# Optimization experiments

Hardware: AMD Instinct MI355X
Metric: run time of the kernel (lower is better)

The kernel has to match this reference:

```python
import jax, jax.numpy as jnp
import numpy as np

N = 100000   # nodes
E = 3200000  # edges
CY = 128     # channels_y (signal length per node)
HID = 10     # hidden_channels
H = 2        # heads
C = 10       # out channels per head
BN_EPS = 1e-5


def _glorot(k, shape):
    lim = float(np.sqrt(6.0 / (shape[0] + shape[1])))
    return jax.random.uniform(k, shape, jnp.float32, -lim, lim)


def setup_inputs() -> dict:
    key = jax.random.key(0)
    ks = jax.random.split(key, 16)
    p = {}
    p["signal"] = jax.random.normal(ks[0], (N, CY), jnp.float32)
    p["edge_index"] = jax.random.randint(ks[1], (2, E), 0, N)
    p["edge_weight"] = jax.random.uniform(ks[2], (E,), jnp.float32)
    p["mask"] = jax.random.bernoulli(ks[3], 0.3, (N,))
    # mlp_in: Linear(CY,512) -> BatchNorm -> ReLU -> Linear(512,HID) (PyG MLP, plain_last)
    p["W1"] = _glorot(ks[4], (CY, 512)); p["b1"] = jnp.zeros((512,), jnp.float32)
    p["gamma"] = jnp.ones((512,), jnp.float32); p["beta"] = jnp.zeros((512,), jnp.float32)
    p["W2"] = _glorot(ks[5], (512, HID)); p["b2"] = jnp.zeros((HID,), jnp.float32)
    # GATv2Conv(HID, HID, heads=2, edge_dim=1, concat=True)
    p["Wl"] = _glorot(ks[6], (HID, H * C)); p["bl"] = jnp.zeros((H * C,), jnp.float32)
    p["Wr"] = _glorot(ks[7], (HID, H * C)); p["br"] = jnp.zeros((H * C,), jnp.float32)
    p["We"] = _glorot(ks[8], (1, H * C))              # lin_edge, no bias
    p["att"] = _glorot(ks[9], (H, C))                 # attention vector per head
    p["gat_bias"] = jnp.zeros((H * C,), jnp.float32)
    # mlp_out: MLP([20,512]) single layer, plain_last -> just Linear (dropout off in eval)
    p["W3"] = _glorot(ks[10], (H * C, 512)); p["b3"] = jnp.zeros((512,), jnp.float32)
    # out_linear: Linear(512, CY)
    p["W4"] = _glorot(ks[11], (512, CY)); p["b4"] = jnp.zeros((CY,), jnp.float32)
    return p


def _forward(signal, edge_index, edge_weight, mask,
             W1, b1, gamma, beta, W2, b2,
             Wl, bl, Wr, br, We, att, gat_bias,
             W3, b3, W4, b4):
    # node masking: (signal.T * ~mask).T
    x = signal * (~mask)[:, None].astype(signal.dtype)
    # mlp_in (eval mode: BN with running mean=0, var=1)
    x = x @ W1 + b1
    x = x * (gamma / jnp.sqrt(jnp.asarray(1.0 + BN_EPS, x.dtype))) + beta
    x = jax.nn.relu(x)
    x = x @ W2 + b2                                   # [N, HID]
    # GATv2Conv
    src, dst = edge_index[0], edge_index[1]
    xl = (x @ Wl + bl).reshape(N, H, C)               # source transform
    xr = (x @ Wr + br).reshape(N, H, C)               # target transform
    ea = (edge_weight[:, None] @ We).reshape(E, H, C)  # edge feature transform
    e = jax.nn.leaky_relu(xl[src] + xr[dst] + ea, 0.2)  # [E,H,C]
    alpha = jnp.einsum('ehc,hc->eh', e, att)          # [E,H]
    # segment softmax over incoming edges of each dst node
    m = jax.ops.segment_max(alpha, dst, num_segments=N)
    ex = jnp.exp(alpha - m[dst])
    den = jax.ops.segment_sum(ex, dst, num_segments=N)
    a = ex / (den[dst] + 1e-16)                       # [E,H]
    out = jax.ops.segment_sum(xl[src] * a[:, :, None], dst, num_segments=N)
    out = out.reshape(N, H * C) + gat_bias            # concat heads + bias
    # mlp_out (single plain-last layer) + out_linear
    out = out @ W3 + b3
    out = out @ W4 + b4
    return out


def reference(signal, edge_index, edge_weight, mask,
              W1, b1, gamma, beta, W2, b2,
              Wl, bl, Wr, br, We, att, gat_bias,
              W3, b3, W4, b4):
    return _forward(signal, edge_index, edge_weight, mask,
                    W1, b1, gamma, beta, W2, b2,
                    Wl, bl, Wr, br, We, att, gat_bias,
                    W3, b3, W4, b4)
```

## Files before the change

### kernel.cpp

```cpp
#include <hip/hip_runtime.h>
#include <hip/hip_bf16.h>

constexpr int NN = 100000;
constexpr int NE = 3200000;
constexpr int CYC = 128;
constexpr int NB = 1563;
constexpr int EBLK = 256;
constexpr int ECHUNK = NE / EBLK;
constexpr int MSCAN = NB * EBLK;
constexpr int CAP = 2432;
constexpr int NBLK_A = (NN + 63) / 64;

#define OFF_W1T    0u
#define OFF_W2T    131072u
#define OFF_B1E    147456u
#define OFF_SMALL  149504u
#define OFF_W34    151808u
#define OFF_B34    162048u
#define OFF_FLAGS  162560u
#define OFF_XLB    163840u
#define OFF_XR     6563840u
#define OFF_GH     14563840u
#define OFF_BB     16164352u
#define OFF_BS     16170752u
#define OFF_BIN    16171776u

#define SF_WLR 0
#define SF_BLR 400
#define SF_ATT 440
#define SF_WE  460
#define SF_GB  480
#define SF_B2  500

typedef __attribute__((ext_vector_type(8))) short bf16x8;
typedef __attribute__((ext_vector_type(4))) float f32x4;

__device__ __forceinline__ float bfu(unsigned short x) {
  return __uint_as_float(((unsigned)x) << 16);
}
__device__ __forceinline__ short f2bf(float f) {
  __hip_bfloat16 h = __float2bfloat16(f);
  return *reinterpret_cast<short*>(&h);
}
__device__ __forceinline__ float LD(const void* p, long i, int f32f) {
  return f32f ? ((const float*)p)[i] : bfu(((const unsigned short*)p)[i]);
}

__global__ __launch_bounds__(256) void kPrep(
    const void* __restrict__ W1, const void* __restrict__ b1,
    const void* __restrict__ gamma, const void* __restrict__ beta,
    const void* __restrict__ W2, const void* __restrict__ b2,
    const void* __restrict__ Wl, const void* __restrict__ bl,
    const void* __restrict__ Wr, const void* __restrict__ br,
    const void* __restrict__ We, const void* __restrict__ att,
    const void* __restrict__ gbias, const void* __restrict__ W3,
    const void* __restrict__ b3, const void* __restrict__ W4,
    const void* __restrict__ b4, const void* __restrict__ mask,
    int* __restrict__ flags,
    short* __restrict__ W1T, float* __restrict__ b1eff, short* __restrict__ W2T,
    float* __restrict__ smallf, float* __restrict__ W34, float* __restrict__ b34)
{
  __shared__ int sfl[2];
  int t = threadIdx.x;
  if (t < 64) {
    const unsigned short* W1u = (const unsigned short*)W1;
    const unsigned* masku = (const unsigned*)mask;
    int big = 0;
#pragma unroll
    for (int k = 0; k < 8; k++) {
      unsigned e = (W1u[t * 8 + k] >> 7) & 0xFF;
      if (e >= 170) big++;
    }
    int byt = 0;
#pragma unroll
    for (int k = 0; k < 4; k++) if (masku[t * 4 + k] & ~1u) byt = 1;
#pragma unroll
    for (int o = 1; o < 64; o <<= 1) {
      big += __shfl_xor(big, o);
      byt |= __shfl_xor(byt, o);
    }
    if (t == 0) {
      sfl[0] = (big >= 4) ? 1 : 0;
      sfl[1] = byt;
      if (blockIdx.x == 0) { flags[0] = sfl[0]; flags[1] = byt; }
    }
  }
  __syncthreads();
  const int f32f = sfl[0];

  int tid = blockIdx.x * 256 + t;
  const float rs = 0.999995000037f;
  if (tid < 65536) {
    int j = tid >> 7, k = tid & 127;
    float s = LD(gamma, j, f32f) * rs;
    W1T[j * 128 + k] = f2bf(LD(W1, k * 512 + j, f32f) * s);
    if (k == 0) b1eff[j] = LD(b1, j, f32f) * s + LD(beta, j, f32f);
  } else if (tid < 73728) {
    int i = tid - 65536;
    int c = i >> 9, k = i & 511;
    W2T[c * 512 + k] = (c < 10) ? f2bf(LD(W2, k * 10 + c, f32f)) : (short)0;
  } else if (tid < 76288) {
    int i = tid - 73728;
    int j = i >> 7, tt = i & 127;
    float acc = 0.f;
    for (int k = 0; k < 512; k++) acc += LD(W3, j * 512 + k, f32f) * LD(W4, k * 128 + tt, f32f);
    W34[j * 128 + tt] = acc;
  } else if (tid < 76416) {
    int tt = tid - 76288;
    float acc = LD(b4, tt, f32f);
    for (int k = 0; k < 512; k++) acc += LD(b3, k, f32f) * LD(W4, k * 128 + tt, f32f);
    b34[tt] = acc;
  } else if (tid < 76932) {
    int i = tid - 76416;
    if (i < 400) {
      int c = i / 40, o = i % 40;
      smallf[SF_WLR + i] = (o < 20) ? LD(Wl, c * 20 + o, f32f) : LD(Wr, c * 20 + (o - 20), f32f);
    } else if (i < 440) {
      int o = i - 400;
      smallf[SF_BLR + o] = (o < 20) ? LD(bl, o, f32f) : LD(br, o - 20, f32f);
    } else if (i < 460) {
      smallf[SF_ATT + (i - 440)] = LD(att, i - 440, f32f);
    } else if (i < 480) {
      smallf[SF_WE + (i - 460)] = LD(We, i - 460, f32f);
    } else if (i < 500) {
      smallf[SF_GB + (i - 480)] = LD(gbias, i - 480, f32f);
    } else {
      int c = i - 500;
      smallf[SF_B2 + c] = (c < 10) ? LD(b2, c, f32f) : 0.f;
    }
  }
}

__global__ __launch_bounds__(256, 2) void kA(
    const void* __restrict__ sig, const void* __restrict__ mask,
    const short* __restrict__ W1T, const float* __restrict__ b1eff,
    const short* __restrict__ W2T, const float* __restrict__ smallf,
    const int* __restrict__ flags,
    unsigned short* __restrict__ xlb, float* __restrict__ xr)
{
  __shared__ __align__(16) char sR1[17408];
  __shared__ short sH[4][32 * 136];
  __shared__ float sb1[512];
  __shared__ float sxh[64][12];
  __shared__ float sWlr[400];
  __shared__ float sblr[40];
  __shared__ float sb2[16];

  short (*sA)[136]        = (short (*)[136])sR1;
  float (*sxhp)[64][17]   = (float (*)[64][17])sR1;
  float (*sxlr)[40]       = (float (*)[40])sR1;

  const int f32f = flags[0];
  const int mk8  = flags[1];
  int t = threadIdx.x;
  int w = t >> 6, l = t & 63;
  int lrow = l & 15, quad = l >> 4;
  int row0 = blockIdx.x * 64;

  for (int i = t; i < 512; i += 256) sb1[i] = b1eff[i];
  for (int i = t; i < 400; i += 256) sWlr[i] = smallf[SF_WLR + i];
  if (t < 40) sblr[t] = smallf[SF_BLR + t];
  if (t < 16) sb2[t] = smallf[SF_B2 + t];

  bf16x8 zz = {0, 0, 0, 0, 0, 0, 0, 0};
#pragma unroll
  for (int k = 0; k < 4; k++) {
    int idx = t + k * 256;
    int row = idx >> 4, seg = idx & 15;
    int gr = row0 + row;
    int grc = gr < NN ? gr : NN - 1;
    bool mbit = mk8 ? (((const unsigned char*)mask)[grc] != 0)
                    : (((const int*)mask)[grc] != 0);
    bf16x8 v;
    if (mbit) {
      v = zz;
    } else if (f32f) {
      const float4* Sf = (const float4*)((const float*)sig + (size_t)grc * CYC) + seg * 2;
      float4 x0 = Sf[0], x1 = Sf[1];
      v[0] = f2bf(x0.x); v[1] = f2bf(x0.y); v[2] = f2bf(x0.z); v[3] = f2bf(x0.w);
      v[4] = f2bf(x1.x); v[5] = f2bf(x1.y); v[6] = f2bf(x1.z); v[7] = f2bf(x1.w);
    } else {
      v = ((const bf16x8*)((const unsigned short*)sig + (size_t)grc * CYC))[seg];
    }
    *(bf16x8*)&sA[row][seg * 8] = v;
  }
  __syncthreads();

  float bcol[8];
#pragma unroll
  for (int ct = 0; ct < 8; ct++) bcol[ct] = sb1[w * 128 + ct * 16 + lrow];

  f32x4 acc[4][8];
#pragma unroll
  for (int rf = 0; rf < 4; rf++)
#pragma unroll
    for (int ct = 0; ct < 8; ct++) acc[rf][ct] = (f32x4){0.f, 0.f, 0.f, 0.f};

  const bf16x8* Bp = (const bf16x8*)W1T;
  int bvbase = w * 2048 + lrow * 16 + quad;
#pragma unroll
  for (int kt = 0; kt < 4; kt++) {
    bf16x8 a0 = *(const bf16x8*)&sA[lrow][kt * 32 + quad * 8];
    bf16x8 a1 = *(const bf16x8*)&sA[16 + lrow][kt * 32 + quad * 8];
    bf16x8 a2f = *(const bf16x8*)&sA[32 + lrow][kt * 32 + quad * 8];
    bf16x8 a3 = *(const bf16x8*)&sA[48 + lrow][kt * 32 + quad * 8];
#pragma unroll
    for (int ct = 0; ct < 8; ct++) {
      bf16x8 bv = Bp[bvbase + ct * 256 + kt * 4];
      acc[0][ct] = __builtin_amdgcn_mfma_f32_16x16x32_bf16(a0, bv, acc[0][ct], 0, 0, 0);
      acc[1][ct] = __builtin_amdgcn_mfma_f32_16x16x32_bf16(a1, bv, acc[1][ct], 0, 0, 0);
      acc[2][ct] = __builtin_amdgcn_mfma_f32_16x16x32_bf16(a2f, bv, acc[2][ct], 0, 0, 0);
      acc[3][ct] = __builtin_amdgcn_mfma_f32_16x16x32_bf16(a3, bv, acc[3][ct], 0, 0, 0);
    }
  }
  __syncthreads();

  const bf16x8* B2p = (const bf16x8*)W2T;
  bf16x8 b2v[4];
#pragma unroll
  for (int kt2 = 0; kt2 < 4; kt2++) b2v[kt2] = B2p[lrow * 64 + w * 16 + kt2 * 4 + quad];

  short* hb = &sH[w][0];
#pragma unroll
  for (int hf = 0; hf < 2; hf++) {
#pragma unroll
    for (int rr = 0; rr < 2; rr++) {
      int rf = hf * 2 + rr;
#pragma unroll
      for (int ct = 0; ct < 8; ct++) {
        float bb = bcol[ct];
#pragma unroll
        for (int r = 0; r < 4; r++) {
          float vv = fmaxf(acc[rf][ct][r] + bb, 0.f);
          hb[(rr * 16 + quad * 4 + r) * 136 + ct * 16 + lrow] = f2bf(vv);
        }
      }
    }
    asm volatile("s_waitcnt lgkmcnt(0)" ::: "memory");

    f32x4 a2[2];
    a2[0] = (f32x4){0.f, 0.f, 0.f, 0.f};
    a2[1] = (f32x4){0.f, 0.f, 0.f, 0.f};
#pragma unroll
    for (int kt2 = 0; kt2 < 4; kt2++) {
      bf16x8 x0 = *(const bf16x8*)&hb[lrow * 136 + kt2 * 32 + quad * 8];
      bf16x8 x1 = *(const bf16x8*)&hb[(16 + lrow) * 136 + kt2 * 32 + quad * 8];
      a2[0] = __builtin_amdgcn_mfma_f32_16x16x32_bf16(x0, b2v[kt2], a2[0], 0, 0, 0);
      a2[1] = __builtin_amdgcn_mfma_f32_16x16x32_bf16(x1, b2v[kt2], a2[1], 0, 0, 0);
    }
#pragma unroll
    for (int f = 0; f < 2; f++)
#pragma unroll
      for (int r = 0; r < 4; r++)
        sxhp[w][hf * 32 + f * 16 + quad * 4 + r][lrow] = a2[f][r];
  }
  __syncthreads();

  for (int i = t; i < 640; i += 256) {
    int row = i / 10, c = i - row * 10;
    sxh[row][c] = sxhp[0][row][c] + sxhp[1][row][c] + sxhp[2][row][c] + sxhp[3][row][c] + sb2[c];
  }
  __syncthreads();

  for (int i = t; i < 2560; i += 256) {
    int row = i / 40, o = i - row * 40;
    float v = sblr[o];
#pragma unroll
    for (int c = 0; c < 10; c++) v += sxh[row][c] * sWlr[c * 40 + o];
    sxlr[row][o] = v;
  }
  __syncthreads();

  int nrows = NN - row0; if (nrows > 64) nrows = 64;
  unsigned* xlb32 = (unsigned*)xlb;
#pragma unroll
  for (int k = 0; k < 4; k++) {
    int i = t + k * 256;
    int row = i >> 4, p = i & 15;
    if (row < nrows) {
      int s0 = 2 * p, s1 = 2 * p + 1;
      float lo = (s0 < 10) ? sxlr[row][s0] : (s0 >= 16 && s0 < 26) ? sxlr[row][s0 - 6] : 0.f;
      float hi = (s1 < 10) ? sxlr[row][s1] : (s1 >= 16 && s1 < 26) ? sxlr[row][s1 - 6] : 0.f;
      unsigned u = (unsigned)(unsigned short)f2bf(lo) |
                   ((unsigned)(unsigned short)f2bf(hi) << 16);
      xlb32[(size_t)(row0 + row) * 16 + p] = u;
    }
  }
#pragma unroll
  for (int k = 0; k < 5; k++) {
    int i = t + k * 256;
    int row = i / 20, c = i - row * 20;
    if (row < nrows) xr[(size_t)(row0 + row) * 20 + c] = sxlr[row][20 + c];
  }
}

__global__ __launch_bounds__(256) void kB1(const int* __restrict__ ei,
                                           int* __restrict__ gh) {
  __shared__ int h[NB];
  int t = threadIdx.x, blk = blockIdx.x;
  for (int i = t; i < NB; i += 256) h[i] = 0;
  __syncthreads();
  const int* dst = ei + NE;
  int base = blk * ECHUNK, bend = base + ECHUNK;
  for (int i = base + t; i < bend; i += 256)
    atomicAdd(&h[dst[i] >> 6], 1);
  __syncthreads();
  for (int i = t; i < NB; i += 256) gh[i * EBLK + blk] = h[i];
}

__global__ __launch_bounds__(256) void kS1(const int* __restrict__ gh,
                                           int* __restrict__ ghx,
                                           int* __restrict__ bsum) {
  __shared__ int sS[256];
  int t = threadIdx.x;
  int base = blockIdx.x * 2048 + t * 8;
  int d[8], tsum = 0;
#pragma unroll
  for (int k = 0; k < 8; k++) {
    d[k] = (base + k < MSCAN) ? gh[base + k] : 0;
    tsum += d[k];
  }
  sS[t] = tsum;
  __syncthreads();
  for (int o = 1; o < 256; o <<= 1) {
    int v = (t >= o) ? sS[t - o] : 0;
    __syncthreads();
    sS[t] += v;
    __syncthreads();
  }
  int run = sS[t] - tsum;
#pragma unroll
  for (int k = 0; k < 8; k++) {
    if (base + k < MSCAN) ghx[base + k] = run;
    run += d[k];
  }
  if (t == 255) bsum[blockIdx.x] = sS[255];
}

__global__ __launch_bounds__(256) void kS2(int* __restrict__ bsum, int nb) {
  __shared__ int sS[256];
  int t = threadIdx.x;
  int v = (t < nb) ? bsum[t] : 0;
  sS[t] = v;
  __syncthreads();
  for (int o = 1; o < 256; o <<= 1) {
    int u = (t >= o) ? sS[t - o] : 0;
    __syncthreads();
    sS[t] += u;
    __syncthreads();
  }
  if (t < nb) bsum[t] = sS[t] - v;
}

__global__ __launch_bounds__(256) void kS3(int* __restrict__ gh,
                                           const int* __restrict__ bsum,
                                           int* __restrict__ bb) {
  int i = blockIdx.x * 256 + threadIdx.x;
  int v = gh[i] + bsum[i >> 11];
  gh[i] = v;
  if ((i & 255) == 0) bb[i >> 8] = v;
  if (i == 0) bb[NB] = NE;
}

__global__ __launch_bounds__(256) void kB3(const int* __restrict__ ei,
                                           const void* __restrict__ ew,
                                           const int* __restrict__ flags,
                                           const int* __restrict__ gh,
                                           int2* __restrict__ binned) {
  __shared__ int cur[NB];
  const int f32f = flags[0];
  int t = threadIdx.x, blk = blockIdx.x;
  for (int i = t; i < NB; i += 256) cur[i] = gh[i * EBLK + blk];
  __syncthreads();
  int base = blk * ECHUNK, bend = base + ECHUNK;
  for (int i = base + t; i < bend; i += 256) {
    int s = ei[i], d = ei[NE + i];
    float w = LD(ew, i, f32f);
    int b = d >> 6;
    int pos = atomicAdd(&cur[b], 1);
    binned[pos] = make_int2(s | ((d & 63) << 17), __float_as_int(w));
  }
}

__global__ __launch_bounds__(256) void kSrtAgg(
    const int* __restrict__ bb, const int2* __restrict__ binned,
    const unsigned short* __restrict__ xlb, const float* __restrict__ xr,
    const float* __restrict__ smallf, const float* __restrict__ W34,
    const float* __restrict__ b34, const int* __restrict__ flags,
    void* __restrict__ out)
{
  __shared__ int2  sES[CAP];
  __shared__ float sXr[64 * 20];
  __shared__ float sW[2560];
  __shared__ int   sCnt[64];
  __shared__ int   sPre[64];
  __shared__ int   sStart[64];
  __shared__ int   sCur[64];
  __shared__ float sb[128];
  __shared__ float sAtt[20], sWe[20], sGb[20];

  const int f32f = flags[0];
  int t = threadIdx.x, b = blockIdx.x;
  int node0 = b * 64;

  for (int i = t; i < 2560; i += 256) sW[i] = W34[i];
  for (int i = t; i < 1280; i += 256) {
    int gi = node0 * 20 + i;
    sXr[i] = (gi < NN * 20) ? xr[gi] : 0.f;
  }
  if (t < 128) sb[t] = b34[t];
  if (t < 64) sCnt[t] = 0;
  if (t < 20) { sAtt[t] = smallf[SF_ATT + t]; sWe[t] = smallf[SF_WE + t]; sGb[t] = smallf[SF_GB + t]; }
  __syncthreads();

  int base = bb[b], end = bb[b + 1];
  int ne = end - base;

  for (int i = t; i < ne; i += 256)
    atomicAdd(&sCnt[(unsigned)binned[base + i].x >> 17], 1);
  __syncthreads();

  if (t < 64) sPre[t] = sCnt[t];
  __syncthreads();
  for (int o = 1; o < 64; o <<= 1) {
    int v = 0;
    if (t < 64 && t >= o) v = sPre[t - o];
    __syncthreads();
    if (t < 64) sPre[t] += v;
    __syncthreads();
  }
  if (t < 64) {
    int ex = sPre[t] - sCnt[t];
    sStart[t] = ex;
    sCur[t] = ex;
  }
  __syncthreads();

  for (int i = t; i < ne; i += 256) {
    int2 e = binned[base + i];
    int dl = (unsigned)e.x >> 17;
    int pos = atomicAdd(&sCur[dl], 1);
    if (pos < CAP) sES[pos] = make_int2(e.x & 0x1FFFF, e.y);
  }
  __syncthreads();

  int n = t >> 2, head = (t >> 1) & 1, part = t & 1;
  float xrw[10], attw[10], wew[10];
#pragma unroll
  for (int c = 0; c < 10; c++) {
    xrw[c]  = sXr[n * 20 + head * 10 + c];
    attw[c] = sAtt[head * 10 + c];
    wew[c]  = sWe[head * 10 + c];
  }
  float acc[10];
#pragma unroll
  for (int c = 0; c < 10; c++) acc[c] = 0.f;
  float den = 0.f;
  int s0 = sStart[n];
  int s1 = s0 + sCnt[n];
  if (s1 > CAP) s1 = CAP;
  for (int i = s0 + part; i < s1; i += 2) {
    int2 e = sES[i];
    const unsigned short* p = xlb + (size_t)e.x * 32 + head * 16;
    uint4 q = *(const uint4*)p;
    unsigned q4 = *(const unsigned*)(p + 8);
    float vl[10];
    unsigned qq[5] = {q.x, q.y, q.z, q.w, q4};
#pragma unroll
    for (int k = 0; k < 5; k++) {
      vl[2 * k]     = __uint_as_float(qq[k] << 16);
      vl[2 * k + 1] = __uint_as_float(qq[k] & 0xffff0000u);
    }
    float ww = __int_as_float(e.y);
    float a = 0.f;
#pragma unroll
    for (int c = 0; c < 10; c++) {
      float v = vl[c] + xrw[c] + ww * wew[c];
      v = fmaxf(v, 0.2f * v);
      a += v * attw[c];
    }
    float pp = __expf(a);
    den += pp;
#pragma unroll
    for (int c = 0; c < 10; c++) acc[c] += pp * vl[c];
  }
  den += __shfl_xor(den, 1);
#pragma unroll
  for (int c = 0; c < 10; c++) acc[c] += __shfl_xor(acc[c], 1);

  __syncthreads();
  if (part == 0) {
    float inv = 1.f / (den + 1e-16f);
#pragma unroll
    for (int c = 0; c < 10; c++)
      sXr[n * 20 + head * 10 + c] = acc[c] * inv + sGb[head * 10 + c];
  }
  __syncthreads();

  int col = t & 127, half = t >> 7;
  for (int n2 = half; n2 < 64; n2 += 2) {
    int gn = node0 + n2;
    if (gn >= NN) break;
    float v = sb[col];
    const float* g = &sXr[n2 * 20];
#pragma unroll
    for (int c = 0; c < 20; c++) v += g[c] * sW[c * 128 + col];
    if (f32f) ((float*)out)[(size_t)gn * 128 + col] = v;
    else ((unsigned short*)out)[(size_t)gn * 128 + col] = (unsigned short)f2bf(v);
  }
}

extern "C" void kernel_launch(void* const* d_in, const int* in_sizes, int n_in,
                              void* d_out, int out_size, void* d_ws, size_t ws_size,
                              hipStream_t stream) {
  (void)in_sizes; (void)n_in; (void)out_size; (void)ws_size;
  const void* sig  = d_in[0];
  const int*  ei   = (const int*)d_in[1];
  const void* ew   = d_in[2];
  const void* mask = d_in[3];
  const void* W1   = d_in[4];
  const void* b1   = d_in[5];
  const void* gam  = d_in[6];
  const void* bet  = d_in[7];
  const void* W2   = d_in[8];
  const void* b2   = d_in[9];
  const void* Wl   = d_in[10];
  const void* bl   = d_in[11];
  const void* Wr   = d_in[12];
  const void* br   = d_in[13];
  const void* We   = d_in[14];
  const void* att  = d_in[15];
  const void* gb   = d_in[16];
  const void* W3   = d_in[17];
  const void* b3   = d_in[18];
  const void* W4   = d_in[19];
  const void* b4   = d_in[20];

  char* ws = (char*)d_ws;
  short* W1T    = (short*)(ws + OFF_W1T);
  short* W2T    = (short*)(ws + OFF_W2T);
  float* b1eff  = (float*)(ws + OFF_B1E);
  float* smallf = (float*)(ws + OFF_SMALL);
  float* W34    = (float*)(ws + OFF_W34);
  float* b34    = (float*)(ws + OFF_B34);
  int*   flags  = (int*)(ws + OFF_FLAGS);
  unsigned short* xlb = (unsigned short*)(ws + OFF_XLB);
  float* xr     = (float*)(ws + OFF_XR);
  int*   gh     = (int*)(ws + OFF_GH);
  int*   bb     = (int*)(ws + OFF_BB);
  int*   bsum   = (int*)(ws + OFF_BS);
  int2*  bincsr = (int2*)(ws + OFF_BIN);

  kPrep<<<301, 256, 0, stream>>>(W1, b1, gam, bet, W2, b2, Wl, bl, Wr, br, We, att,
                                 gb, W3, b3, W4, b4, mask, flags,
                                 W1T, b1eff, W2T, smallf, W34, b34);
  kA<<<NBLK_A, 256, 0, stream>>>(sig, mask, W1T, b1eff, W2T, smallf, flags, xlb, xr);
  kB1<<<EBLK, 256, 0, stream>>>(ei, gh);
  kS1<<<(MSCAN + 2047) / 2048, 256, 0, stream>>>(gh, gh, bsum);
  kS2<<<1, 256, 0, stream>>>(bsum, (MSCAN + 2047) / 2048);
  kS3<<<NB, 256, 0, stream>>>(gh, bsum, bb);
  kB3<<<EBLK, 256, 0, stream>>>(ei, ew, flags, gh, bincsr);
  kSrtAgg<<<NB, 256, 0, stream>>>(bb, bincsr, xlb, xr, smallf, W34, b34, flags, d_out);
}
```

Measured before the change: 448.0 us.

## Build per-node CSR with global atomics instead of two-level bin sort

Replaces the block-bucketed histogram, scan and in-LDS per-node sort with a direct per-node global histogram, a scan over node counts, and a global-atomic scatter straight into per-node CSR order. The aggregation kernel then reads edges from global memory by node range, dropping the shared-memory re-sort and its CAP truncation. It also software-prefetches the next edge and its source features. The cost is heavy global atomic contention on per-node counters, and the scatter order within each node is no longer deterministic.

```diff
diff --git a/kernel.cpp b/kernel.cpp
--- a/kernel.cpp
+++ b/kernel.cpp
@@ -5,11 +5,8 @@
 constexpr int NE = 3200000;
 constexpr int CYC = 128;
 constexpr int NB = 1563;
-constexpr int EBLK = 256;
-constexpr int ECHUNK = NE / EBLK;
-constexpr int MSCAN = NB * EBLK;
-constexpr int CAP = 2432;
 constexpr int NBLK_A = (NN + 63) / 64;
+constexpr int NSCAN = 100352;
 
 #define OFF_W1T    0u
 #define OFF_W2T    131072u
@@ -20,8 +17,9 @@
 #define OFF_FLAGS  162560u
 #define OFF_XLB    163840u
 #define OFF_XR     6563840u
-#define OFF_GH     14563840u
-#define OFF_BB     16164352u
+#define OFF_NC     14563840u
+#define OFF_NS     14965248u
+#define OFF_NCU    15366656u
 #define OFF_BS     16170752u
 #define OFF_BIN    16171776u
 
@@ -58,7 +56,8 @@
     const void* __restrict__ b4, const void* __restrict__ mask,
     int* __restrict__ flags,
     short* __restrict__ W1T, float* __restrict__ b1eff, short* __restrict__ W2T,
-    float* __restrict__ smallf, float* __restrict__ W34, float* __restrict__ b34)
+    float* __restrict__ smallf, float* __restrict__ W34, float* __restrict__ b34,
+    int* __restrict__ ncnt)
 {
   __shared__ int sfl[2];
   int t = threadIdx.x;
@@ -89,6 +88,8 @@
   const int f32f = sfl[0];
 
   int tid = blockIdx.x * 256 + t;
+  if (tid < NSCAN) ncnt[tid] = 0;
+
   const float rs = 0.999995000037f;
   if (tid < 65536) {
     int j = tid >> 7, k = tid & 127;
@@ -294,30 +295,24 @@
   }
 }
 
-__global__ __launch_bounds__(256) void kB1(const int* __restrict__ ei,
-                                           int* __restrict__ gh) {
-  __shared__ int h[NB];
-  int t = threadIdx.x, blk = blockIdx.x;
-  for (int i = t; i < NB; i += 256) h[i] = 0;
-  __syncthreads();
+__global__ __launch_bounds__(256) void kHist(const int* __restrict__ ei,
+                                             int* __restrict__ ncnt) {
   const int* dst = ei + NE;
-  int base = blk * ECHUNK, bend = base + ECHUNK;
-  for (int i = base + t; i < bend; i += 256)
-    atomicAdd(&h[dst[i] >> 6], 1);
-  __syncthreads();
-  for (int i = t; i < NB; i += 256) gh[i * EBLK + blk] = h[i];
-}
-
-__global__ __launch_bounds__(256) void kS1(const int* __restrict__ gh,
-                                           int* __restrict__ ghx,
-                                           int* __restrict__ bsum) {
+  int stride = gridDim.x * 256;
+  for (int i = blockIdx.x * 256 + threadIdx.x; i < NE; i += stride)
+    atomicAdd(&ncnt[dst[i]], 1);
+}
+
+__global__ __launch_bounds__(256) void kS1(const int* __restrict__ in,
+                                           int* __restrict__ outx,
+                                           int* __restrict__ bsum, int nelem) {
   __shared__ int sS[256];
   int t = threadIdx.x;
   int base = blockIdx.x * 2048 + t * 8;
   int d[8], tsum = 0;
 #pragma unroll
   for (int k = 0; k < 8; k++) {
-    d[k] = (base + k < MSCAN) ? gh[base + k] : 0;
+    d[k] = (base + k < nelem) ? in[base + k] : 0;
     tsum += d[k];
   }
   sS[t] = tsum;
@@ -331,7 +326,7 @@
   int run = sS[t] - tsum;
 #pragma unroll
   for (int k = 0; k < 8; k++) {
-    if (base + k < MSCAN) ghx[base + k] = run;
+    if (base + k < nelem) outx[base + k] = run;
     run += d[k];
   }
   if (t == 255) bsum[blockIdx.x] = sS[255];
@@ -352,51 +347,43 @@
   if (t < nb) bsum[t] = sS[t] - v;
 }
 
-__global__ __launch_bounds__(256) void kS3(int* __restrict__ gh,
-                                           const int* __restrict__ bsum,
-                                           int* __restrict__ bb) {
+__global__ __launch_bounds__(256) void kS3n(int* __restrict__ nstart,
+                                            const int* __restrict__ bsum,
+                                            int* __restrict__ ncur, int nelem) {
   int i = blockIdx.x * 256 + threadIdx.x;
-  int v = gh[i] + bsum[i >> 11];
-  gh[i] = v;
-  if ((i & 255) == 0) bb[i >> 8] = v;
-  if (i == 0) bb[NB] = NE;
-}
-
-__global__ __launch_bounds__(256) void kB3(const int* __restrict__ ei,
-                                           const void* __restrict__ ew,
-                                           const int* __restrict__ flags,
-                                           const int* __restrict__ gh,
-                                           int2* __restrict__ binned) {
-  __shared__ int cur[NB];
+  if (i < nelem) {
+    int v = nstart[i] + bsum[i >> 11];
+    nstart[i] = v;
+    ncur[i] = v;
+  }
+}
+
+__global__ __launch_bounds__(256) void kB3n(const int* __restrict__ ei,
+                                            const void* __restrict__ ew,
+                                            const int* __restrict__ flags,
+                                            int* __restrict__ ncur,
+                                            int2* __restrict__ binned) {
   const int f32f = flags[0];
-  int t = threadIdx.x, blk = blockIdx.x;
-  for (int i = t; i < NB; i += 256) cur[i] = gh[i * EBLK + blk];
-  __syncthreads();
-  int base = blk * ECHUNK, bend = base + ECHUNK;
-  for (int i = base + t; i < bend; i += 256) {
+  int stride = gridDim.x * 256;
+  for (int i = blockIdx.x * 256 + threadIdx.x; i < NE; i += stride) {
     int s = ei[i], d = ei[NE + i];
     float w = LD(ew, i, f32f);
-    int b = d >> 6;
-    int pos = atomicAdd(&cur[b], 1);
-    binned[pos] = make_int2(s | ((d & 63) << 17), __float_as_int(w));
-  }
-}
-
-__global__ __launch_bounds__(256) void kSrtAgg(
-    const int* __restrict__ bb, const int2* __restrict__ binned,
+    int pos = atomicAdd(&ncur[d], 1);
+    binned[pos] = make_int2(s, __float_as_int(w));
+  }
+}
+
+__global__ __launch_bounds__(256) void kAgg(
+    const int* __restrict__ nstart, const int2* __restrict__ binned,
     const unsigned short* __restrict__ xlb, const float* __restrict__ xr,
     const float* __restrict__ smallf, const float* __restrict__ W34,
     const float* __restrict__ b34, const int* __restrict__ flags,
     void* __restrict__ out)
 {
-  __shared__ int2  sES[CAP];
   __shared__ float sXr[64 * 20];
   __shared__ float sW[2560];
-  __shared__ int   sCnt[64];
-  __shared__ int   sPre[64];
-  __shared__ int   sStart[64];
-  __shared__ int   sCur[64];
   __shared__ float sb[128];
+  __shared__ int   sStart[65];
   __shared__ float sAtt[20], sWe[20], sGb[20];
 
   const int f32f = flags[0];
@@ -409,39 +396,8 @@
     sXr[i] = (gi < NN * 20) ? xr[gi] : 0.f;
   }
   if (t < 128) sb[t] = b34[t];
-  if (t < 64) sCnt[t] = 0;
+  if (t < 65) sStart[t] = nstart[node0 + t];
   if (t < 20) { sAtt[t] = smallf[SF_ATT + t]; sWe[t] = smallf[SF_WE + t]; sGb[t] = smallf[SF_GB + t]; }
-  __syncthreads();
-
-  int base = bb[b], end = bb[b + 1];
-  int ne = end - base;
-
-  for (int i = t; i < ne; i += 256)
-    atomicAdd(&sCnt[(unsigned)binned[base + i].x >> 17], 1);
-  __syncthreads();
-
-  if (t < 64) sPre[t] = sCnt[t];
-  __syncthreads();
-  for (int o = 1; o < 64; o <<= 1) {
-    int v = 0;
-    if (t < 64 && t >= o) v = sPre[t - o];
-    __syncthreads();
-    if (t < 64) sPre[t] += v;
-    __syncthreads();
-  }
-  if (t < 64) {
-    int ex = sPre[t] - sCnt[t];
-    sStart[t] = ex;
-    sCur[t] = ex;
-  }
-  __syncthreads();
-
-  for (int i = t; i < ne; i += 256) {
-    int2 e = binned[base + i];
-    int dl = (unsigned)e.x >> 17;
-    int pos = atomicAdd(&sCur[dl], 1);
-    if (pos < CAP) sES[pos] = make_int2(e.x & 0x1FFFF, e.y);
-  }
   __syncthreads();
 
   int n = t >> 2, head = (t >> 1) & 1, part = t & 1;
@@ -456,14 +412,25 @@
 #pragma unroll
   for (int c = 0; c < 10; c++) acc[c] = 0.f;
   float den = 0.f;
-  int s0 = sStart[n];
-  int s1 = s0 + sCnt[n];
-  if (s1 > CAP) s1 = CAP;
-  for (int i = s0 + part; i < s1; i += 2) {
-    int2 e = sES[i];
+  int s0 = sStart[n], s1 = sStart[n + 1];
+
+  int i = s0 + part;
+  int2 e; uint4 q; unsigned q4;
+  if (i < s1) {
+    e = binned[i];
     const unsigned short* p = xlb + (size_t)e.x * 32 + head * 16;
-    uint4 q = *(const uint4*)p;
-    unsigned q4 = *(const unsigned*)(p + 8);
+    q = *(const uint4*)p;
+    q4 = *(const unsigned*)(p + 8);
+  }
+  while (i < s1) {
+    int j = i + 2;
+    int2 en; uint4 qn; unsigned qn4;
+    if (j < s1) {
+      en = binned[j];
+      const unsigned short* pn = xlb + (size_t)en.x * 32 + head * 16;
+      qn = *(const uint4*)pn;
+      qn4 = *(const unsigned*)(pn + 8);
+    }
     float vl[10];
     unsigned qq[5] = {q.x, q.y, q.z, q.w, q4};
 #pragma unroll
@@ -483,6 +450,7 @@
     den += pp;
 #pragma unroll
     for (int c = 0; c < 10; c++) acc[c] += pp * vl[c];
+    e = en; q = qn; q4 = qn4; i = j;
   }
   den += __shfl_xor(den, 1);
 #pragma unroll
@@ -546,19 +514,20 @@
   int*   flags  = (int*)(ws + OFF_FLAGS);
   unsigned short* xlb = (unsigned short*)(ws + OFF_XLB);
   float* xr     = (float*)(ws + OFF_XR);
-  int*   gh     = (int*)(ws + OFF_GH);
-  int*   bb     = (int*)(ws + OFF_BB);
+  int*   ncnt   = (int*)(ws + OFF_NC);
+  int*   nstart = (int*)(ws + OFF_NS);
+  int*   ncur   = (int*)(ws + OFF_NCU);
   int*   bsum   = (int*)(ws + OFF_BS);
   int2*  bincsr = (int2*)(ws + OFF_BIN);
 
-  kPrep<<<301, 256, 0, stream>>>(W1, b1, gam, bet, W2, b2, Wl, bl, Wr, br, We, att,
+  kPrep<<<392, 256, 0, stream>>>(W1, b1, gam, bet, W2, b2, Wl, bl, Wr, br, We, att,
                                  gb, W3, b3, W4, b4, mask, flags,
-                                 W1T, b1eff, W2T, smallf, W34, b34);
+                                 W1T, b1eff, W2T, smallf, W34, b34, ncnt);
+  kHist<<<2048, 256, 0, stream>>>(ei, ncnt);
   kA<<<NBLK_A, 256, 0, stream>>>(sig, mask, W1T, b1eff, W2T, smallf, flags, xlb, xr);
-  kB1<<<EBLK, 256, 0, stream>>>(ei, gh);
-  kS1<<<(MSCAN + 2047) / 2048, 256, 0, stream>>>(gh, gh, bsum);
-  kS2<<<1, 256, 0, stream>>>(bsum, (MSCAN + 2047) / 2048);
-  kS3<<<NB, 256, 0, stream>>>(gh, bsum, bb);
-  kB3<<<EBLK, 256, 0, stream>>>(ei, ew, flags, gh, bincsr);
-  kSrtAgg<<<NB, 256, 0, stream>>>(bb, bincsr, xlb, xr, smallf, W34, b34, flags, d_out);
-}
+  kS1<<<(NSCAN + 2047) / 2048, 256, 0, stream>>>(ncnt, nstart, bsum, NSCAN);
+  kS2<<<1, 256, 0, stream>>>(bsum, (NSCAN + 2047) / 2048);
+  kS3n<<<(NSCAN + 255) / 256, 256, 0, stream>>>(nstart, bsum, ncur, NSCAN);
+  kB3n<<<2048, 256, 0, stream>>>(ei, ew, flags, ncur, bincsr);
+  kAgg<<<NB, 256, 0, stream>>>(nstart, bincsr, xlb, xr, smallf, W34, b34, flags, d_out);
+}
```

Result: slower. 729.7 us (+62.9%).
